# Kernel optimization log

Measured on AMD Instinct MI355X. Metric: run time of the kernel, lower is better.

Reference implementation:

```python
import jax, jax.numpy as jnp
import numpy as np

# ---- module constants (from init_kwargs) ----
N_POLES = 80          # N -> dictionary width 2N+1 = 161
T_SEQ = 36            # T
LAM_F = 0.1           # lam_f
RMIN, RMAX = 0.8, 1.1 # r_r
TMIN, TMAX = 0.1, np.pi  # r_t
NSAMPLE, DDATA = 128, 50
MAX_ITER = 100


def real_D(T, rho, theta):
    # CONSTR=True path: clamp poles into the valid annulus/sector
    rho = jnp.clip(rho, RMIN, RMAX)
    theta = jnp.clip(theta, TMIN, TMAX)
    i = jnp.arange(T, dtype=rho.dtype)[:, None]            # [T,1]
    p = jnp.power(rho[None, :], i)                          # [T,N] rho^i
    W1 = p * jnp.cos(i * theta[None, :])                    # [T,N]
    W2 = p * jnp.sin(i * theta[None, :])                    # [T,N]
    ones = jnp.ones((T, 1), dtype=rho.dtype)
    return jnp.concatenate([ones, W1, W2], axis=1)          # [T, 2N+1]


def fista_reweighted(D, Y, lambd, w, max_iter=MAX_ITER):
    # D: [T,Np], Y: [n,T,d], w: [n,Np,d]
    Np = D.shape[1]
    DtD = D.T @ D                                           # [Np,Np]
    DtY = jnp.einsum('tp,ntd->npd', D, Y)                   # [n,Np,d]
    L = jnp.linalg.norm(DtD, ord=2)                         # spectral norm
    Linv = 1.0 / L
    wl = w * (lambd * Linv)
    A = jnp.eye(Np, dtype=D.dtype) - DtD * Linv             # [Np,Np]
    c_minus = DtY * Linv - wl
    c_plus = DtY * Linv + wl
    x0 = jnp.zeros_like(DtY)

    def step(carry, _):
        x, y, t, done = carry
        Ay = jnp.einsum('pq,nqd->npd', A, y)
        # soft-threshold via max/min split (as in source)
        x_new = jnp.maximum(Ay + c_minus, 0.0) + jnp.minimum(Ay + c_plus, 0.0)
        t_new = (1.0 + jnp.sqrt(1.0 + 4.0 * t * t)) / 2.0
        tt = (t - 1.0) / t_new
        y_new = x_new + tt * (x_new - x)
        conv = jnp.linalg.norm(x - x_new) / Np < 1e-5       # global check
        x_o = jnp.where(done, x, x_new)
        y_o = jnp.where(done, y, y_new)
        t_o = jnp.where(done, t, t_new)
        return (x_o, y_o, t_o, done | conv), None

    step = jax.checkpoint(step)
    init = (x0, x0, jnp.asarray(1.0, D.dtype), jnp.asarray(False))
    (x, _, _, _), _ = jax.lax.scan(step, init, None, length=max_iter)
    return x


def rh_fista(D, Y, lam):
    Np = D.shape[1]
    w = jnp.ones((Y.shape[0], Np, Y.shape[2]), dtype=Y.dtype)
    C = None
    for _ in range(2):  # fixed 2 reweighting rounds, as in source
        C = fista_reweighted(D, Y, lam, w)
        w_raw = 1.0 / (jnp.abs(C) + 0.01)
        w = w_raw / jnp.sum(jnp.abs(w_raw), axis=1, keepdims=True) * Np
    R = jnp.einsum('tp,npd->ntd', D, C)
    return C, D, R


def setup_inputs() -> dict:
    key = jax.random.key(0)
    k1, k2, k3 = jax.random.split(key, 3)
    x = jax.random.normal(k1, (NSAMPLE, T_SEQ, DDATA), dtype=jnp.float32)
    rho = jax.random.uniform(k2, (N_POLES,), dtype=jnp.float32) * (RMAX - RMIN) + RMIN
    theta = jax.random.uniform(k3, (N_POLES,), dtype=jnp.float32) * (TMAX - TMIN) + TMIN
    return {"x": x, "rho": rho, "theta": theta}


def reference(x, rho, theta):
    D = real_D(T_SEQ, rho, theta)            # [T, 2N+1]
    C, D, R = rh_fista(D, x, LAM_F)          # wiRH=True path
    return C, D, R
```

## Files before the change

### kernel.cpp

```cpp
#include <hip/hip_runtime.h>
#include <math.h>

#define NPOLES 80
#define NP 161
#define NPAD 164
#define TSEQ 36
#define NSAMP 128
#define DDATA 50
#define LAMF 0.1f
#define NPD (NP*DDATA)
#define TD (TSEQ*DDATA)
#define CSIZE (NSAMP*NPD)
#define RSIZE (NSAMP*TD)
#define DSIZE (TSEQ*NP)

#define RT_N 11
#define KC_N 5
#define FRAG_CHUNK 512
#define YK 168

typedef __attribute__((ext_vector_type(8))) short s8b;
typedef __attribute__((ext_vector_type(4))) float f4;

__device__ __forceinline__ unsigned short f2b(float f) {
    unsigned u = __float_as_uint(f);
    unsigned r = (u + 0x7FFFu + ((u >> 16) & 1u)) >> 16;
    return (unsigned short)r;
}
__device__ __forceinline__ float b2f(unsigned short h) {
    return __uint_as_float(((unsigned)h) << 16);
}

__global__ void k_build_D(const float* __restrict__ rho, const float* __restrict__ theta,
                          float* __restrict__ Dw, float* __restrict__ Dout) {
    int idx = blockIdx.x * 256 + threadIdx.x;
    if (idx >= DSIZE) return;
    int t = idx / NP, p = idx - (idx / NP) * NP;
    float v;
    if (p == 0) {
        v = 1.f;
    } else {
        int j = (p <= NPOLES) ? (p - 1) : (p - 1 - NPOLES);
        float r  = fminf(fmaxf(rho[j],   0.8f), 1.1f);
        float th = fminf(fmaxf(theta[j], 0.1f), 3.14159265358979323846f);
        double pw  = pow((double)r, (double)t);
        double ang = (double)t * (double)th;
        v = (float)(pw * ((p <= NPOLES) ? cos(ang) : sin(ang)));
    }
    Dw[idx] = v;
    Dout[idx] = v;
}

__global__ void k_ddt(const float* __restrict__ Dw, float* __restrict__ DDt) {
    int idx = blockIdx.x * 256 + threadIdx.x;
    if (idx >= TSEQ * TSEQ) return;
    int i = idx / TSEQ, j = idx - (idx / TSEQ) * TSEQ;
    float acc = 0.f;
    for (int p = 0; p < NP; ++p) acc = fmaf(Dw[i * NP + p], Dw[j * NP + p], acc);
    DDt[idx] = acc;
}

__global__ void k_power(const float* __restrict__ DDt, float* __restrict__ scal) {
    __shared__ float sM[TSEQ * TSEQ];
    __shared__ float sv[TSEQ];
    int tid = threadIdx.x;
    for (int i = tid; i < TSEQ * TSEQ; i += 64) sM[i] = DDt[i];
    if (tid < TSEQ) sv[tid] = 1.f;
    __syncthreads();
    for (int it = 0; it < 150; ++it) {
        float u = 0.f;
        if (tid < TSEQ) {
            for (int q = 0; q < TSEQ; ++q) u = fmaf(sM[tid * TSEQ + q], sv[q], u);
        }
        float nn = u * u;
        for (int o = 32; o > 0; o >>= 1) nn += __shfl_down(nn, o);
        nn = __shfl(nn, 0);
        float inv = rsqrtf(nn);
        __syncthreads();
        if (tid < TSEQ) sv[tid] = u * inv;
        __syncthreads();
    }
    float rq = 0.f;
    if (tid < TSEQ) {
        float uu = 0.f;
        for (int q = 0; q < TSEQ; ++q) uu = fmaf(sM[tid * TSEQ + q], sv[q], uu);
        rq = uu * sv[tid];
    }
    for (int o = 32; o > 0; o >>= 1) rq += __shfl_down(rq, o);
    if (tid == 0) { scal[0] = 1.f / rq; scal[1] = rq; }
}

__global__ void k_A(const float* __restrict__ Dw, const float* __restrict__ scal,
                    float* __restrict__ Apad) {
    int idx = blockIdx.x * 256 + threadIdx.x;
    if (idx >= NP * NPAD) return;
    int q = idx / NPAD, p = idx - (idx / NPAD) * NPAD;
    float v = 0.f;
    if (p < NP) {
        float acc = 0.f;
        for (int t = 0; t < TSEQ; ++t) acc = fmaf(Dw[t * NP + q], Dw[t * NP + p], acc);
        v = ((p == q) ? 1.f : 0.f) - acc * scal[0];
    }
    Apad[idx] = v;
}

__global__ void k_dty(const float* __restrict__ Dw, const float* __restrict__ Y,
                      float* __restrict__ dty) {
    int idx = blockIdx.x * 256 + threadIdx.x;
    if (idx >= CSIZE) return;
    int n = idx / NPD;
    int r = idx - n * NPD;
    int p = r / DDATA;
    int d = r - p * DDATA;
    const float* yp = Y + n * TD + d;
    float acc = 0.f;
    for (int t = 0; t < TSEQ; ++t) acc = fmaf(Dw[t * NP + p], yp[t * DDATA], acc);
    dty[idx] = acc;
}

__global__ void k_Afrag(const float* __restrict__ Apad,
                        short* __restrict__ AfH, short* __restrict__ AfL) {
    int idx = blockIdx.x * 256 + threadIdx.x;
    if (idx >= RT_N * KC_N * 64) return;
    int lane = idx & 63;
    int chunk = idx >> 6;
    int kc = chunk % KC_N;
    int rt = chunk / KC_N;
    int p = rt * 16 + (lane & 15);
    int q0 = kc * 32 + (lane >> 4) * 8;
    int base = chunk * FRAG_CHUNK + lane * 8;
#pragma unroll
    for (int j = 0; j < 8; ++j) {
        int q = q0 + j;
        float v = (p < NP && q < NP) ? Apad[q * NPAD + p] : 0.f;
        unsigned short h = f2b(v);
        float rem = v - b2f(h);
        AfH[base + j] = (short)h;
        AfL[base + j] = (short)f2b(rem);
    }
}

__global__ __launch_bounds__(256, 2) void k_fista(
    const float* __restrict__ Apad,
    const s8b* __restrict__ AfH, const s8b* __restrict__ AfL,
    const float* __restrict__ dty_g, const float* __restrict__ scal,
    float* __restrict__ Cout)
{
    __shared__ unsigned short Yh[2][16][YK];
    __shared__ unsigned short Yl[2][16][YK];
    __shared__ float yrem[2][16];
    __shared__ float colpart[4][16];
    __shared__ float sS[16];

    const int tid = threadIdx.x;
    const int n  = blockIdx.x >> 2;
    const int dq = blockIdx.x & 3;
    const int w = tid >> 6;
    const int lane = tid & 63;
    const int c0 = lane & 15;
    const int g = lane >> 4;
    const int rt0 = w * 3;
    const int ntr = (w == 3) ? 2 : 3;
    const int ncol = (dq == 3) ? 11 : 13;
    const int colv = dq * 13 + c0;
    const bool cvalid = c0 < ncol;
    const float Linv = scal[0];
    const float lamL = LAMF * Linv;

    s8b ahr[3][KC_N], alr[3][KC_N];
    const s8b zer = {0, 0, 0, 0, 0, 0, 0, 0};
#pragma unroll
    for (int rr = 0; rr < 3; ++rr) {
#pragma unroll
        for (int kc = 0; kc < KC_N; ++kc) {
            if (rr < ntr) {
                int ck = (rt0 + rr) * KC_N + kc;
                ahr[rr][kc] = AfH[ck * 64 + lane];
                alr[rr][kc] = AfL[ck * 64 + lane];
            } else {
                ahr[rr][kc] = zer;
                alr[rr][kc] = zer;
            }
        }
    }

    int rowb[3];
    float dtL[3][4];
    f4 a160r[3];
#pragma unroll
    for (int rr = 0; rr < 3; ++rr) {
        rowb[rr] = (rt0 + rr) * 16 + g * 4;
#pragma unroll
        for (int r = 0; r < 4; ++r) {
            int row = rowb[rr] + r;
            float v = 0.f;
            if ((rr < ntr) && row < NP && cvalid)
                v = dty_g[n * NPD + row * DDATA + colv];
            dtL[rr][r] = v * Linv;
            a160r[rr][r] = ((rr < ntr) && row < NP) ? Apad[160 * NPAD + row] : 0.f;
        }
    }

    float x_[3][4], wlam_[3][4];
#pragma unroll
    for (int rr = 0; rr < 3; ++rr)
#pragma unroll
        for (int r = 0; r < 4; ++r) wlam_[rr][r] = lamL;

#pragma unroll 1
    for (int round = 0; round < 2; ++round) {
#pragma unroll
        for (int rr = 0; rr < 3; ++rr)
#pragma unroll
            for (int r = 0; r < 4; ++r) x_[rr][r] = 0.f;
        {
            unsigned* ph = (unsigned*)&Yh[0][0][0];
            unsigned* pl = (unsigned*)&Yl[0][0][0];
            for (int i = tid; i < 16 * YK / 2; i += 256) { ph[i] = 0u; pl[i] = 0u; }
            if (tid < 16) yrem[0][tid] = 0.f;
        }
        float tmom = 1.f;
        int cur = 0;
        __syncthreads();

#pragma unroll 1
        for (int it = 0; it < 100; ++it) {
            float tn = (1.f + sqrtf(fmaf(4.f * tmom, tmom, 1.f))) * 0.5f;
            float ttc = (tmom - 1.f) / tn;
            tmom = tn;
            const int nxt = cur ^ 1;

            f4 acc[3];
#pragma unroll
            for (int rr = 0; rr < 3; ++rr)
#pragma unroll
                for (int r = 0; r < 4; ++r) acc[rr][r] = dtL[rr][r];

#pragma unroll
            for (int kc = 0; kc < KC_N; ++kc) {
                int yo = kc * 32 + g * 8;
                s8b bh = *(const s8b*)&Yh[cur][c0][yo];
                s8b bl = *(const s8b*)&Yl[cur][c0][yo];
#pragma unroll
                for (int rr = 0; rr < 3; ++rr) {
                    if (rr < ntr) {
                        acc[rr] = __builtin_amdgcn_mfma_f32_16x16x32_bf16(ahr[rr][kc], bh, acc[rr], 0, 0, 0);
                        acc[rr] = __builtin_amdgcn_mfma_f32_16x16x32_bf16(ahr[rr][kc], bl, acc[rr], 0, 0, 0);
                        acc[rr] = __builtin_amdgcn_mfma_f32_16x16x32_bf16(alr[rr][kc], bh, acc[rr], 0, 0, 0);
                    }
                }
            }
            {
                float yv = yrem[cur][c0];
#pragma unroll
                for (int rr = 0; rr < 3; ++rr)
                    if (rr < ntr)
#pragma unroll
                        for (int r = 0; r < 4; ++r)
                            acc[rr][r] = fmaf(a160r[rr][r], yv, acc[rr][r]);
            }

#pragma unroll
            for (int rr = 0; rr < 3; ++rr) {
                if (rr < ntr) {
                    unsigned yb[4], rb[4];
                    float yn0 = 0.f;
#pragma unroll
                    for (int r = 0; r < 4; ++r) {
                        float bb = acc[rr][r];
                        float wl = wlam_[rr][r];
                        float cl = fminf(fmaxf(bb, -wl), wl);
                        float xn = bb - cl;
                        float yn = fmaf(ttc, xn - x_[rr][r], xn);
                        x_[rr][r] = xn;
                        if (r == 0) yn0 = yn;
                        unsigned u = __float_as_uint(yn);
                        yb[r] = u;
                        rb[r] = __float_as_uint(yn - __uint_as_float(u & 0xFFFF0000u));
                    }
                    int rt = rt0 + rr;
                    if (rt < 10) {
                        uint2 hp, lp;
                        hp.x = __builtin_amdgcn_perm(yb[1], yb[0], 0x07060302u);
                        hp.y = __builtin_amdgcn_perm(yb[3], yb[2], 0x07060302u);
                        lp.x = __builtin_amdgcn_perm(rb[1], rb[0], 0x07060302u);
                        lp.y = __builtin_amdgcn_perm(rb[3], rb[2], 0x07060302u);
                        *(uint2*)&Yh[nxt][c0][rowb[rr]] = hp;
                        *(uint2*)&Yl[nxt][c0][rowb[rr]] = lp;
                    } else if (g == 0) {
                        yrem[nxt][c0] = yn0;
                    }
                }
            }
            __syncthreads();
            cur = nxt;
        }

        if (round == 0) {
            float ps = 0.f;
#pragma unroll
            for (int rr = 0; rr < 3; ++rr) {
                if (rr < ntr) {
#pragma unroll
                    for (int r = 0; r < 4; ++r) {
                        if (rowb[rr] + r < NP)
                            ps += 1.f / (fabsf(x_[rr][r]) + 0.01f);
                    }
                }
            }
            ps += __shfl_xor(ps, 16);
            ps += __shfl_xor(ps, 32);
            if (lane < 16) colpart[w][lane] = ps;
            __syncthreads();
            if (tid < 16) {
                float s = colpart[0][tid] + colpart[1][tid] + colpart[2][tid] + colpart[3][tid];
                sS[tid] = (float)NP / s;
            }
            __syncthreads();
            float sc = sS[c0] * lamL;
#pragma unroll
            for (int rr = 0; rr < 3; ++rr)
#pragma unroll
                for (int r = 0; r < 4; ++r)
                    wlam_[rr][r] = (1.f / (fabsf(x_[rr][r]) + 0.01f)) * sc;
            __syncthreads();
        }
    }

#pragma unroll
    for (int rr = 0; rr < 3; ++rr) {
        if ((rr < ntr) && cvalid) {
#pragma unroll
            for (int r = 0; r < 4; ++r) {
                int row = rowb[rr] + r;
                if (row < NP)
                    Cout[n * NPD + row * DDATA + colv] = x_[rr][r];
            }
        }
    }
}

__global__ void k_R(const float* __restrict__ Dw, const float* __restrict__ Cf,
                    float* __restrict__ Rout) {
    int idx = blockIdx.x * 256 + threadIdx.x;
    if (idx >= RSIZE) return;
    int n = idx / TD;
    int r = idx - n * TD;
    int t = r / DDATA;
    int d = r - t * DDATA;
    const float* xp = Cf + n * NPD + d;
    float acc = 0.f;
    for (int p = 0; p < NP; ++p) acc = fmaf(Dw[t * NP + p], xp[p * DDATA], acc);
    Rout[idx] = acc;
}

extern "C" void kernel_launch(void* const* d_in, const int* in_sizes, int n_in,
                              void* d_out, int out_size, void* d_ws, size_t ws_size,
                              hipStream_t stream) {
    const float* Y     = (const float*)d_in[0];
    const float* rho   = (const float*)d_in[1];
    const float* theta = (const float*)d_in[2];
    float* Cout = (float*)d_out;
    float* Dout = Cout + CSIZE;
    float* Rout = Dout + DSIZE;

    float* ws    = (float*)d_ws;
    float* Dw    = ws;
    float* Apad  = Dw + 5824;
    float* DDt   = Apad + 26416;
    float* scal  = DDt + 1312;
    float* dty   = scal + 16;
    float* AfH_f = dty + CSIZE;
    float* AfL_f = AfH_f + 14080;

    k_build_D<<<(DSIZE + 255) / 256, 256, 0, stream>>>(rho, theta, Dw, Dout);
    k_ddt<<<(TSEQ * TSEQ + 255) / 256, 256, 0, stream>>>(Dw, DDt);
    k_power<<<1, 64, 0, stream>>>(DDt, scal);
    k_A<<<(NP * NPAD + 255) / 256, 256, 0, stream>>>(Dw, scal, Apad);
    k_dty<<<(CSIZE + 255) / 256, 256, 0, stream>>>(Dw, Y, dty);
    k_Afrag<<<(RT_N * KC_N * 64 + 255) / 256, 256, 0, stream>>>(Apad, (short*)AfH_f, (short*)AfL_f);

    k_fista<<<NSAMP * 4, 256, 0, stream>>>(Apad, (const s8b*)AfH_f, (const s8b*)AfL_f,
                                           dty, scal, Cout);

    k_R<<<(RSIZE + 255) / 256, 256, 0, stream>>>(Dw, Cout, Rout);
}
```

Before: 394.8 us.

## Relayout shared Y buffers for conflict-free LDS, precompute momentum table, raise MFMA priority

The hi/lo bf16 halves of the shared Y iterate are moved into one interleaved byte buffer. Each lane now reads and writes 8-byte pieces at fixed strides, which is meant to remove LDS bank conflicts on the MFMA B-operand loads and on the writebacks. The FISTA momentum coefficients are computed once in the power-iteration kernel and read from a global table, so the per-iteration sqrt and divide go away. s_setprio brackets the MFMA section to favour matrix issue across waves. The costs are extra scalar loads from global memory and split 8-byte LDS reads instead of 16-byte ones.

```diff
diff --git a/kernel.cpp b/kernel.cpp
--- a/kernel.cpp
+++ b/kernel.cpp
@@ -17,10 +17,13 @@
 #define RT_N 11
 #define KC_N 5
 #define FRAG_CHUNK 512
-#define YK 168
+
+#define YBUF 10240
 
 typedef __attribute__((ext_vector_type(8))) short s8b;
 typedef __attribute__((ext_vector_type(4))) float f4;
+
+struct u2x2 { uint2 a, b; };
 
 __device__ __forceinline__ unsigned short f2b(float f) {
     unsigned u = __float_as_uint(f);
@@ -60,10 +63,19 @@
     DDt[idx] = acc;
 }
 
-__global__ void k_power(const float* __restrict__ DDt, float* __restrict__ scal) {
+__global__ void k_power(const float* __restrict__ DDt, float* __restrict__ scal,
+                        float* __restrict__ ttab) {
     __shared__ float sM[TSEQ * TSEQ];
     __shared__ float sv[TSEQ];
     int tid = threadIdx.x;
+    if (tid == 0) {
+        float t = 1.f;
+        for (int k = 0; k < 100; ++k) {
+            float tn = (1.f + sqrtf(fmaf(4.f * t, t, 1.f))) * 0.5f;
+            ttab[k] = (t - 1.f) / tn;
+            t = tn;
+        }
+    }
     for (int i = tid; i < TSEQ * TSEQ; i += 64) sM[i] = DDt[i];
     if (tid < TSEQ) sv[tid] = 1.f;
     __syncthreads();
@@ -144,11 +156,10 @@
     const float* __restrict__ Apad,
     const s8b* __restrict__ AfH, const s8b* __restrict__ AfL,
     const float* __restrict__ dty_g, const float* __restrict__ scal,
-    float* __restrict__ Cout)
+    const float* __restrict__ ttab, float* __restrict__ Cout)
 {
-    __shared__ unsigned short Yh[2][16][YK];
-    __shared__ unsigned short Yl[2][16][YK];
-    __shared__ float yrem[2][16];
+    __shared__ char Yb[2 * YBUF];
+    __shared__ float yremf[2][16];
     __shared__ float colpart[4][16];
     __shared__ float sS[16];
 
@@ -167,6 +178,9 @@
     const float Linv = scal[0];
     const float lamL = LAMF * Linv;
 
+    const int rdbase = (c0 << 3) + (g << 9);
+    const int wrbase = (c0 << 3);
+
     s8b ahr[3][KC_N], alr[3][KC_N];
     const s8b zer = {0, 0, 0, 0, 0, 0, 0, 0};
 #pragma unroll
@@ -214,21 +228,19 @@
 #pragma unroll
             for (int r = 0; r < 4; ++r) x_[rr][r] = 0.f;
         {
-            unsigned* ph = (unsigned*)&Yh[0][0][0];
-            unsigned* pl = (unsigned*)&Yl[0][0][0];
-            for (int i = tid; i < 16 * YK / 2; i += 256) { ph[i] = 0u; pl[i] = 0u; }
-            if (tid < 16) yrem[0][tid] = 0.f;
-        }
-        float tmom = 1.f;
+            unsigned* pz = (unsigned*)Yb;
+            for (int i = tid; i < YBUF / 4; i += 256) pz[i] = 0u;
+            if (tid < 16) yremf[0][tid] = 0.f;
+        }
         int cur = 0;
         __syncthreads();
 
 #pragma unroll 1
         for (int it = 0; it < 100; ++it) {
-            float tn = (1.f + sqrtf(fmaf(4.f * tmom, tmom, 1.f))) * 0.5f;
-            float ttc = (tmom - 1.f) / tn;
-            tmom = tn;
+            const float ttc = ttab[it];
             const int nxt = cur ^ 1;
+            const char* rp = Yb + cur * YBUF + rdbase;
+            char* wp = Yb + nxt * YBUF + wrbase;
 
             f4 acc[3];
 #pragma unroll
@@ -236,11 +248,17 @@
 #pragma unroll
                 for (int r = 0; r < 4; ++r) acc[rr][r] = dtL[rr][r];
 
+            __builtin_amdgcn_s_setprio(1);
 #pragma unroll
             for (int kc = 0; kc < KC_N; ++kc) {
-                int yo = kc * 32 + g * 8;
-                s8b bh = *(const s8b*)&Yh[cur][c0][yo];
-                s8b bl = *(const s8b*)&Yl[cur][c0][yo];
+                const char* p = rp + kc * 2048;
+                u2x2 hh2, ll2;
+                hh2.a = *(const uint2*)(p);
+                hh2.b = *(const uint2*)(p + 256);
+                ll2.a = *(const uint2*)(p + 128);
+                ll2.b = *(const uint2*)(p + 384);
+                s8b bh = __builtin_bit_cast(s8b, hh2);
+                s8b bl = __builtin_bit_cast(s8b, ll2);
 #pragma unroll
                 for (int rr = 0; rr < 3; ++rr) {
                     if (rr < ntr) {
@@ -251,7 +269,7 @@
                 }
             }
             {
-                float yv = yrem[cur][c0];
+                float yv = yremf[cur][c0];
 #pragma unroll
                 for (int rr = 0; rr < 3; ++rr)
                     if (rr < ntr)
@@ -259,11 +277,12 @@
                         for (int r = 0; r < 4; ++r)
                             acc[rr][r] = fmaf(a160r[rr][r], yv, acc[rr][r]);
             }
+            __builtin_amdgcn_s_setprio(0);
 
 #pragma unroll
             for (int rr = 0; rr < 3; ++rr) {
                 if (rr < ntr) {
-                    unsigned yb[4], rb[4];
+                    unsigned yb4[4], rb4[4];
                     float yn0 = 0.f;
 #pragma unroll
                     for (int r = 0; r < 4; ++r) {
@@ -275,20 +294,21 @@
                         x_[rr][r] = xn;
                         if (r == 0) yn0 = yn;
                         unsigned u = __float_as_uint(yn);
-                        yb[r] = u;
-                        rb[r] = __float_as_uint(yn - __uint_as_float(u & 0xFFFF0000u));
+                        yb4[r] = u;
+                        rb4[r] = __float_as_uint(yn - __uint_as_float(u & 0xFFFF0000u));
                     }
                     int rt = rt0 + rr;
                     if (rt < 10) {
                         uint2 hp, lp;
-                        hp.x = __builtin_amdgcn_perm(yb[1], yb[0], 0x07060302u);
-                        hp.y = __builtin_amdgcn_perm(yb[3], yb[2], 0x07060302u);
-                        lp.x = __builtin_amdgcn_perm(rb[1], rb[0], 0x07060302u);
-                        lp.y = __builtin_amdgcn_perm(rb[3], rb[2], 0x07060302u);
-                        *(uint2*)&Yh[nxt][c0][rowb[rr]] = hp;
-                        *(uint2*)&Yl[nxt][c0][rowb[rr]] = lp;
+                        hp.x = __builtin_amdgcn_perm(yb4[1], yb4[0], 0x07060302u);
+                        hp.y = __builtin_amdgcn_perm(yb4[3], yb4[2], 0x07060302u);
+                        lp.x = __builtin_amdgcn_perm(rb4[1], rb4[0], 0x07060302u);
+                        lp.y = __builtin_amdgcn_perm(rb4[3], rb4[2], 0x07060302u);
+                        char* q = wp + (rt * 4 + g) * 256;
+                        *(uint2*)(q)       = hp;
+                        *(uint2*)(q + 128) = lp;
                     } else if (g == 0) {
-                        yrem[nxt][c0] = yn0;
+                        yremf[nxt][c0] = yn0;
                     }
                 }
             }
@@ -369,19 +389,20 @@
     float* Apad  = Dw + 5824;
     float* DDt   = Apad + 26416;
     float* scal  = DDt + 1312;
-    float* dty   = scal + 16;
+    float* ttabd = scal + 16;
+    float* dty   = ttabd + 112;
     float* AfH_f = dty + CSIZE;
     float* AfL_f = AfH_f + 14080;
 
     k_build_D<<<(DSIZE + 255) / 256, 256, 0, stream>>>(rho, theta, Dw, Dout);
     k_ddt<<<(TSEQ * TSEQ + 255) / 256, 256, 0, stream>>>(Dw, DDt);
-    k_power<<<1, 64, 0, stream>>>(DDt, scal);
+    k_power<<<1, 64, 0, stream>>>(DDt, scal, ttabd);
     k_A<<<(NP * NPAD + 255) / 256, 256, 0, stream>>>(Dw, scal, Apad);
     k_dty<<<(CSIZE + 255) / 256, 256, 0, stream>>>(Dw, Y, dty);
     k_Afrag<<<(RT_N * KC_N * 64 + 255) / 256, 256, 0, stream>>>(Apad, (short*)AfH_f, (short*)AfL_f);
 
     k_fista<<<NSAMP * 4, 256, 0, stream>>>(Apad, (const s8b*)AfH_f, (const s8b*)AfL_f,
-                                           dty, scal, Cout);
+                                           dty, scal, ttabd, Cout);
 
     k_R<<<(RSIZE + 255) / 256, 256, 0, stream>>>(Dw, Cout, Rout);
 }
```

Measured after the change: 392.2 us. No clear change (-0.7%).
